# Kernel optimization log

Hardware: AMD Instinct MI355X
Metric: run time of the kernel (lower is better)

## Reference

```python
import jax, jax.numpy as jnp
import numpy as np

EPS = 1e-5

def conv1x1(x, W, b):
    # x: (B,C,H,W), W: (O,C), b: (O,)
    return jnp.einsum('bchw,oc->bohw', x, W) + b[None, :, None, None]

def setup_inputs() -> dict:
    key = jax.random.key(0)
    ks = jax.random.split(key, 16)
    B, C_in, C1, D, K, H, Wd = 8, 512, 256, 128, 32, 96, 96
    s = lambda k, shape, fan: jax.random.normal(k, shape, jnp.float32) * (1.0 / np.sqrt(fan))
    return {
        'X': jax.random.normal(ks[0], (B, C_in, H, Wd), jnp.float32),
        'W_theta': s(ks[1], (C1, C_in), C_in), 'b_theta': jnp.zeros((C1,), jnp.float32),
        'W_phi': s(ks[2], (C1, C_in), C_in), 'b_phi': jnp.zeros((C1,), jnp.float32),
        'W_g': s(ks[3], (C1, C_in), C_in), 'b_g': jnp.zeros((C1,), jnp.float32),
        'W2': s(ks[4], (C_in, C1), C1), 'b2': jnp.zeros((C_in,), jnp.float32),
        'W3': s(ks[5], (D, C_in), C_in), 'b3': jnp.zeros((D,), jnp.float32),
        'codewords': jax.random.normal(ks[6], (K, D), jnp.float32),
        'scale': -jax.random.uniform(ks[7], (K,), jnp.float32),  # Deep-TEN init: U(-1,0)
        'W_fc': s(ks[8], (C_in, D), D), 'b_fc': jnp.zeros((C_in,), jnp.float32),
    }

def reference(X, W_theta, b_theta, W_phi, b_phi, W_g, b_g, W2, b2, W3, b3,
              codewords, scale, W_fc, b_fc):
    B, C_in, H, Wd = X.shape
    C1 = W_theta.shape[0]
    D, K = W3.shape[0], codewords.shape[0]
    N = H * Wd
    # --- non-local (channel-attention) block ---
    theta = conv1x1(X, W_theta, b_theta).reshape(B, C1, N)          # (B,C1,N)
    phi = conv1x1(X, W_phi, b_phi).reshape(B, C1, N)                # (B,C1,N)
    g = conv1x1(X, W_g, b_g).reshape(B, C1, N)                      # (B,C1,N)
    f = jax.nn.softmax(jnp.einsum('bcn,bdn->bcd', theta, phi), axis=-1)  # (B,C1,C1)
    y = jnp.einsum('bcd,bdn->bcn', f, g).reshape(B, C1, H, Wd)
    z = conv1x1(y, W2, b2) + X                                      # (B,C_in,H,W)
    # --- Deep-TEN encoding ---
    z_ = conv1x1(z, W3, b3)                                         # (B,D,H,W)
    x = z_.reshape(B, D, N).transpose(0, 2, 1)                      # (B,N,D)
    # squared L2 distances to codewords without (B,N,K,D) residuals
    dist = (jnp.sum(x * x, -1, keepdims=True)
            - 2.0 * jnp.einsum('bnd,kd->bnk', x, codewords)
            + jnp.sum(codewords * codewords, -1))                   # (B,N,K)
    A = jax.nn.softmax(scale * dist, axis=-1)                       # (B,N,K)
    # E_k = sum_i A_ik (x_i - c_k)
    E = jnp.einsum('bnk,bnd->bkd', A, x) - A.sum(1)[..., None] * codewords  # (B,K,D)
    # --- training-mode batch norm over K channels (no affine) ---
    mean = E.mean(axis=(0, 2), keepdims=True)
    var = E.var(axis=(0, 2), keepdims=True)
    e = jax.nn.relu((E - mean) * jax.lax.rsqrt(var + EPS))
    Es = e.sum(axis=1)                                              # (B,D)
    gamma = jax.nn.sigmoid(Es @ W_fc.T + b_fc)                      # (B,C_in)
    return z * gamma[:, :, None, None]
```

## Files before the change

### kernel.cpp

```cpp
#include <hip/hip_runtime.h>


typedef unsigned short u16;

#define Bb 8
#define Cc 512
#define C1 256
#define Dd 128
#define Kk 32
#define Nn 9216

typedef __attribute__((ext_vector_type(8))) short short8v;
typedef __attribute__((ext_vector_type(4))) short short4v;
typedef __attribute__((ext_vector_type(4))) float f32x4;

__device__ __forceinline__ float b2f(u16 u) {
  union { unsigned int i; float f; } v; v.i = ((unsigned int)u) << 16; return v.f;
}
__device__ __forceinline__ u16 f2b(float f) {
  union { float f; unsigned int i; } v; v.f = f;
  unsigned int x = v.i;
  return (u16)((x + 0x7fffu + ((x >> 16) & 1u)) >> 16);
}

__device__ __forceinline__ float b2fOrF(float x) { return x; }
__device__ __forceinline__ float b2fOrF(u16 x) { return b2f(x); }

__device__ __forceinline__ float4 load4(const float* p) { return *(const float4*)p; }
__device__ __forceinline__ float4 load4(const u16* p) {
  ushort4 q = *(const ushort4*)p;
  return make_float4(b2f(q.x), b2f(q.y), b2f(q.z), b2f(q.w));
}
__device__ __forceinline__ void store4(float* p, float a, float b, float c, float d) {
  *(float4*)p = make_float4(a, b, c, d);
}

__device__ __forceinline__ float waveSum(float v) {
  #pragma unroll
  for (int o = 32; o > 0; o >>= 1) v += __shfl_xor(v, o);
  return v;
}
__device__ __forceinline__ float waveMax(float v) {
  #pragma unroll
  for (int o = 32; o > 0; o >>= 1) v = fmaxf(v, __shfl_xor(v, o));
  return v;
}
__device__ __forceinline__ float blockSum256(float v) {
  __shared__ float sm[4];
  v = waveSum(v);
  if ((threadIdx.x & 63) == 0) sm[threadIdx.x >> 6] = v;
  __syncthreads();
  float r = sm[0] + sm[1] + sm[2] + sm[3];
  __syncthreads();
  return r;
}
__device__ __forceinline__ float blockMax256(float v) {
  __shared__ float sm[4];
  v = waveMax(v);
  if ((threadIdx.x & 63) == 0) sm[threadIdx.x >> 6] = v;
  __syncthreads();
  float r = fmaxf(fmaxf(sm[0], sm[1]), fmaxf(sm[2], sm[3]));
  __syncthreads();
  return r;
}

__device__ __forceinline__ f32x4 mfma_bf16_16x16x32(short8v a, short8v b, f32x4 c) {
  asm("v_mfma_f32_16x16x32_bf16 %0, %1, %2, %0" : "+v"(c) : "v"(a), "v"(b));
  return c;
}

__device__ __forceinline__ int fsw(int r) { return (r ^ (r >> 2) ^ (r >> 4)) & 3; }

__device__ __forceinline__ void cvt2(float x0, float x1, unsigned int& h, unsigned int& l) {
  asm("v_cvt_pk_bf16_f32 %0, %1, %2" : "=v"(h) : "v"(x0), "v"(x1));
  union { unsigned int u; float f; } fa, fb;
  fa.u = h << 16; fb.u = h & 0xffff0000u;
  float r0 = x0 - fa.f, r1 = x1 - fb.f;
  asm("v_cvt_pk_bf16_f32 %0, %1, %2" : "=v"(l) : "v"(r0), "v"(r1));
}

__device__ __forceinline__ void storeC(float* p, float v) { *p = v; }
__device__ __forceinline__ void storeC(u16* p, float v) { *p = f2b(v); }

template<typename TO, int NF, bool TRANSB, bool ATOMIC>
__global__ __launch_bounds__(256, 2) void gemm_mfma(
    const float* __restrict__ A, const float* __restrict__ B, TO* __restrict__ C,
    int N, int K,
    long long sA, long long sB, long long sC,
    const float* __restrict__ biasRow, long long sBias,
    int kChunk, int numKS, int gnx, int gny)
{
  static_assert(NF == 4 || NF == 8, "NF");
  static_assert(!TRANSB || NF == 4, "TRANSB tile assumes BN==128");
  static_assert(!ATOMIC || __is_same(TO, float), "atomic path is fp32");
  constexpr int BN = 32 * NF;
  __shared__ __align__(16) u16 Asm_[2][128][40];
  __shared__ __align__(16) u16 Bsm_[2][BN][40];

  int id = blockIdx.x;
  {
    const int nwg = gridDim.x;
    if ((nwg & 7) == 0) id = (id & 7) * (nwg >> 3) + (id >> 3);
  }
  const int per = gnx * gny;
  const int bz = id / per;
  const int rem = id - bz * per;
  const int by = rem % gny;
  const int bx = rem / gny;
  const int b = bz / numKS, ks = bz - b * numKS;
  A += b * sA; B += b * sB; C += b * sC;
  const int m0 = by * 128, n0 = bx * BN;
  const int kBeg = ks * kChunk;
  const int kEnd = (kBeg + kChunk < K) ? (kBeg + kChunk) : K;

  const int t = threadIdx.x;
  const int w = t >> 6, lane = t & 63;
  const int wr = w >> 1, wc = w & 1;
  const int lr = lane & 15, lq = lane >> 4;

  const int sar = t >> 1, sak = (t & 1) * 16;
  const int kg = t >> 5, ng = t & 31;

  float ra[16];
  float rb[32];

  auto loadA = [&](int k0) {
    const float* p = A + (long long)(m0 + sar) * K + (k0 + sak);
    #pragma unroll
    for (int i = 0; i < 4; ++i) {
      float4 v = *(const float4*)(p + i * 4);
      ra[i*4+0] = v.x; ra[i*4+1] = v.y; ra[i*4+2] = v.z; ra[i*4+3] = v.w;
    }
  };
  auto loadB = [&](int k0) {
    if constexpr (TRANSB) {
      const float* p = B + (long long)(n0 + sar) * K + (k0 + sak);
      #pragma unroll
      for (int i = 0; i < 4; ++i) {
        float4 v = *(const float4*)(p + i * 4);
        rb[i*4+0] = v.x; rb[i*4+1] = v.y; rb[i*4+2] = v.z; rb[i*4+3] = v.w;
      }
    } else {
      const float* p = B + (long long)(k0 + kg * 4) * N + (n0 + ng * 8);
      #pragma unroll
      for (int i = 0; i < 4; ++i) {
        float4 v0 = *(const float4*)(p + (long long)i * N);
        float4 v1 = *(const float4*)(p + (long long)i * N + 4);
        rb[i*8+0]=v0.x; rb[i*8+1]=v0.y; rb[i*8+2]=v0.z; rb[i*8+3]=v0.w;
        rb[i*8+4]=v1.x; rb[i*8+5]=v1.y; rb[i*8+6]=v1.z; rb[i*8+7]=v1.w;
      }
    }
  };

  auto pack8row = [&](const float* s8, u16 (&dstH)[40], u16 (&dstL)[40], int col) {
    union { unsigned int u[4]; short8v v; } H, L;
    #pragma unroll
    for (int p = 0; p < 4; ++p) cvt2(s8[2*p], s8[2*p+1], H.u[p], L.u[p]);
    *(short8v*)&dstH[col] = H.v;
    *(short8v*)&dstL[col] = L.v;
  };

  auto stage = [&]() {
    {
      const int f = fsw(sar);
      #pragma unroll
      for (int h = 0; h < 2; ++h) {
        const int col = ((((sak >> 3) + h) ^ f) << 3);
        pack8row(&ra[h*8], Asm_[0][sar], Asm_[1][sar], col);
      }
    }
    if constexpr (TRANSB) {
      const int f = fsw(sar);
      #pragma unroll
      for (int h = 0; h < 2; ++h) {
        const int col = ((((sak >> 3) + h) ^ f) << 3);
        pack8row(&rb[h*8], Bsm_[0][sar], Bsm_[1][sar], col);
      }
    } else {
      #pragma unroll
      for (int j = 0; j < 8; ++j) {
        const int n = ng * 8 + j;
        const int col = (((kg >> 1) ^ fsw(n)) << 3) + (kg & 1) * 4;
        union { unsigned int u[2]; short4v v; } H, L;
        #pragma unroll
        for (int p = 0; p < 2; ++p)
          cvt2(rb[(2*p)*8 + j], rb[(2*p+1)*8 + j], H.u[p], L.u[p]);
        *(short4v*)&Bsm_[0][n][col] = H.v;
        *(short4v*)&Bsm_[1][n][col] = L.v;
      }
    }
  };

  f32x4 acc[4][NF];
  #pragma unroll
  for (int im = 0; im < 4; ++im)
    #pragma unroll
    for (int in = 0; in < NF; ++in)
      acc[im][in] = f32x4{0.f, 0.f, 0.f, 0.f};

  loadA(kBeg); loadB(kBeg);
  for (int k0 = kBeg; k0 < kEnd; k0 += 32) {
    stage();
    if (k0 + 32 < kEnd) { loadA(k0 + 32); loadB(k0 + 32); }
    __syncthreads();
    short8v af[2][4];
    #pragma unroll
    for (int im = 0; im < 4; ++im) {
      const int r = wr * 64 + im * 16 + lr;
      const int col = ((lq ^ fsw(r)) << 3);
      af[0][im] = *(const short8v*)&Asm_[0][r][col];
      af[1][im] = *(const short8v*)&Asm_[1][r][col];
    }
    #pragma unroll
    for (int in = 0; in < NF; ++in) {
      const int rB = wc * NF * 16 + in * 16 + lr;
      const int colB = ((lq ^ fsw(rB)) << 3);
      short8v bh = *(const short8v*)&Bsm_[0][rB][colB];
      short8v bl = *(const short8v*)&Bsm_[1][rB][colB];
      #pragma unroll
      for (int im = 0; im < 4; ++im) {
        acc[im][in] = mfma_bf16_16x16x32(af[0][im], bh, acc[im][in]);
        acc[im][in] = mfma_bf16_16x16x32(af[0][im], bl, acc[im][in]);
        acc[im][in] = mfma_bf16_16x16x32(af[1][im], bh, acc[im][in]);
      }
    }
    __syncthreads();
  }
  asm volatile("s_nop 7\n\ts_nop 7\n\ts_nop 7");

  #pragma unroll
  for (int im = 0; im < 4; ++im) {
    #pragma unroll
    for (int in = 0; in < NF; ++in) {
      const f32x4 a = acc[im][in];
      const int gc = n0 + wc * NF * 16 + in * 16 + lr;
      #pragma unroll
      for (int p = 0; p < 4; ++p) {
        const int gr = m0 + wr * 64 + im * 16 + lq * 4 + p;
        const long long idx = (long long)gr * N + gc;
        if constexpr (ATOMIC) {
          atomicAdd(&C[idx], a[p]);
        } else {
          float v = a[p];
          if (biasRow) v += biasRow[b * sBias + gr];
          storeC(&C[idx], v);
        }
      }
    }
  }
}

template<bool TRANSB>
__global__ __launch_bounds__(256) void gemm64(
    const float* __restrict__ A, const float* __restrict__ B, float* __restrict__ C,
    int M, int N, int K,
    long long sA, long long sB, long long sC,
    const float* __restrict__ biasRow, long long sBias)
{
  const int bz = blockIdx.z;
  A += (long long)bz * sA;
  B += (long long)bz * sB;
  C += (long long)bz * sC;
  const int m0 = blockIdx.y * 64, n0 = blockIdx.x * 64;
  __shared__ __align__(16) float As[16][64];
  __shared__ __align__(16) float Bs[16][64];
  const int t = threadIdx.x;
  const int lr = t >> 2, lk = (t & 3) << 2;
  const int tm = (t >> 4) << 2, tn = (t & 15) << 2;
  float acc[4][4] = {};
  for (int k0 = 0; k0 < K; k0 += 16) {
    {
      float4 a = load4(A + (long long)(m0 + lr) * K + (k0 + lk));
      As[lk + 0][lr] = a.x; As[lk + 1][lr] = a.y; As[lk + 2][lr] = a.z; As[lk + 3][lr] = a.w;
    }
    if (TRANSB) {
      float4 b = load4(B + (long long)(n0 + lr) * K + (k0 + lk));
      Bs[lk + 0][lr] = b.x; Bs[lk + 1][lr] = b.y; Bs[lk + 2][lr] = b.z; Bs[lk + 3][lr] = b.w;
    } else {
      const int kr = t >> 4, nc = (t & 15) << 2;
      float4 b = load4(B + (long long)(k0 + kr) * N + (n0 + nc));
      *(float4*)&Bs[kr][nc] = b;
    }
    __syncthreads();
    #pragma unroll
    for (int kk = 0; kk < 16; ++kk) {
      const float4 av = *(const float4*)&As[kk][tm];
      const float4 bv = *(const float4*)&Bs[kk][tn];
      acc[0][0] = fmaf(av.x, bv.x, acc[0][0]);
      acc[0][1] = fmaf(av.x, bv.y, acc[0][1]);
      acc[0][2] = fmaf(av.x, bv.z, acc[0][2]);
      acc[0][3] = fmaf(av.x, bv.w, acc[0][3]);
      acc[1][0] = fmaf(av.y, bv.x, acc[1][0]);
      acc[1][1] = fmaf(av.y, bv.y, acc[1][1]);
      acc[1][2] = fmaf(av.y, bv.z, acc[1][2]);
      acc[1][3] = fmaf(av.y, bv.w, acc[1][3]);
      acc[2][0] = fmaf(av.z, bv.x, acc[2][0]);
      acc[2][1] = fmaf(av.z, bv.y, acc[2][1]);
      acc[2][2] = fmaf(av.z, bv.z, acc[2][2]);
      acc[2][3] = fmaf(av.z, bv.w, acc[2][3]);
      acc[3][0] = fmaf(av.w, bv.x, acc[3][0]);
      acc[3][1] = fmaf(av.w, bv.y, acc[3][1]);
      acc[3][2] = fmaf(av.w, bv.z, acc[3][2]);
      acc[3][3] = fmaf(av.w, bv.w, acc[3][3]);
    }
    __syncthreads();
  }
  #pragma unroll
  for (int i = 0; i < 4; ++i) {
    const int m = m0 + tm + i;
    float bias = biasRow ? biasRow[bz * sBias + m] : 0.f;
    store4(C + (long long)m * N + (n0 + tn),
           acc[i][0] + bias, acc[i][1] + bias, acc[i][2] + bias, acc[i][3] + bias);
  }
}

__global__ __launch_bounds__(256) void rowsum_kernel(const float* __restrict__ X,
                                                     float* __restrict__ s, int N) {
  long long row = blockIdx.x;
  const float* p = X + row * N;
  float acc = 0.f;
  for (int i = threadIdx.x; i < N; i += 256) acc += p[i];
  acc = blockSum256(acc);
  if (threadIdx.x == 0) s[row] = acc;
}

__global__ __launch_bounds__(256) void gemv512_kernel(const float* __restrict__ W,
                                                      const float* __restrict__ s,
                                                      float* __restrict__ out) {
  int b = blockIdx.x;
  __shared__ float ssm[Cc];
  for (int i = threadIdx.x; i < Cc; i += 256) ssm[i] = s[b * Cc + i];
  __syncthreads();
  int i = threadIdx.x;
  const float* wr = W + i * Cc;
  float acc = 0.f;
  for (int k = 0; k < Cc; ++k) acc = fmaf(wr[k], ssm[k], acc);
  out[b * C1 + i] = acc;
}

__global__ __launch_bounds__(256) void softmax_kernel(float* __restrict__ L,
    const float* __restrict__ bth, const float* __restrict__ bph,
    const float* __restrict__ u, const float* __restrict__ v) {
  int row = blockIdx.x;
  int b = row >> 8, i = row & 255;
  int j = threadIdx.x;
  float bt = bth[i], bp = bph[j];
  long long idx = (long long)row * C1 + j;
  float val = L[idx] + bt * v[b * C1 + j] + u[b * C1 + i] * bp + (float)Nn * bt * bp;
  float mx = blockMax256(val);
  float p = expf(val - mx);
  float sm = blockSum256(p);
  L[idx] = p / sm;
}

__global__ __launch_bounds__(256) void w_kernel(const float* __restrict__ f,
                                                const float* __restrict__ bg,
                                                float* __restrict__ w) {
  int b = blockIdx.x;
  __shared__ float bgs[C1];
  bgs[threadIdx.x] = bg[threadIdx.x];
  __syncthreads();
  int i = threadIdx.x;
  const float* fr = f + ((long long)b * C1 + i) * C1;
  float acc = 0.f;
  for (int j = 0; j < C1; ++j) acc = fmaf(fr[j], bgs[j], acc);
  w[b * C1 + i] = acc;
}

__global__ __launch_bounds__(256) void q_kernel(const float* __restrict__ W2,
                                                const float* __restrict__ b2v,
                                                const float* __restrict__ w,
                                                float* __restrict__ q) {
  int gi = blockIdx.x * 256 + threadIdx.x;
  int b = gi >> 9, c = gi & 511;
  __shared__ float wsm[C1];
  wsm[threadIdx.x] = w[b * C1 + threadIdx.x];
  __syncthreads();
  const float* wr = W2 + c * C1;
  float acc = b2v[c];
  for (int i = 0; i < C1; ++i) acc = fmaf(wr[i], wsm[i], acc);
  q[gi] = acc;
}

__global__ __launch_bounds__(256) void adddiag_kernel(float* __restrict__ P) {
  int gi = blockIdx.x * 256 + threadIdx.x;
  int b = gi >> 9, c = gi & 511;
  P[((long long)b * Cc + c) * Cc + c] += 1.f;
}

__global__ __launch_bounds__(256) void zqbias_kernel(const float* __restrict__ W3,
    const float* __restrict__ b3, const float* __restrict__ q, float* __restrict__ zqb) {
  int gi = blockIdx.x * 256 + threadIdx.x;
  int b = gi >> 7, d = gi & 127;
  const float* wr = W3 + d * Cc;
  const float* qr = q + b * Cc;
  float acc = b3[d];
  for (int c = 0; c < Cc; ++c) acc = fmaf(wr[c], qr[c], acc);
  zqb[gi] = acc;
}

template<typename ZT>
__global__ __launch_bounds__(256) void enc_kernel(
    const ZT* __restrict__ zq,
    const float* __restrict__ cw,
    const float* __restrict__ sc,
    float* __restrict__ Eraw,
    float* __restrict__ Asum)
{
  __shared__ float csm[Kk][Dd + 1];
  __shared__ float cc[Kk], ssm[Kk];
  __shared__ float sA[Kk][256 + 1];
  __shared__ float zs[Dd][17];
  const int tid = threadIdx.x;
  const int b = blockIdx.y;
  const int n0 = blockIdx.x * 256;

  #pragma unroll
  for (int r = 0; r < 16; ++r) {
    int idx = r * 256 + tid;
    csm[idx >> 7][idx & 127] = cw[idx];
  }
  if (tid < Kk) ssm[tid] = sc[tid];
  __syncthreads();
  if (tid < Kk) {
    float a = 0.f;
    for (int d = 0; d < Dd; ++d) { float cv = csm[tid][d]; a = fmaf(cv, cv, a); }
    cc[tid] = a;
  }
  __syncthreads();

  const int n = n0 + tid;
  const ZT* zp = zq + (long long)b * Dd * Nn + n;
  float dots[Kk];
  #pragma unroll
  for (int k = 0; k < Kk; ++k) dots[k] = 0.f;
  float xx = 0.f;
  for (int d = 0; d < Dd; ++d) {
    float xv = b2fOrF(zp[(long long)d * Nn]);
    xx = fmaf(xv, xv, xx);
    #pragma unroll
    for (int k = 0; k < Kk; ++k) dots[k] = fmaf(csm[k][d], xv, dots[k]);
  }
  float mx = -1e30f;
  #pragma unroll
  for (int k = 0; k < Kk; ++k) {
    float l = ssm[k] * (xx - 2.f * dots[k] + cc[k]);
    dots[k] = l;
    mx = fmaxf(mx, l);
  }
  float sum = 0.f;
  #pragma unroll
  for (int k = 0; k < Kk; ++k) { float p = expf(dots[k] - mx); dots[k] = p; sum += p; }
  float inv = 1.f / sum;
  #pragma unroll
  for (int k = 0; k < Kk; ++k) sA[k][tid] = dots[k] * inv;
  __syncthreads();
  if (tid < Kk) {
    float s = 0.f;
    for (int p = 0; p < 256; ++p) s += sA[tid][p];
    atomicAdd(&Asum[b * Kk + tid], s);
  }

  float acc[16];
  #pragma unroll
  for (int j = 0; j < 16; ++j) acc[j] = 0.f;
  const int k = tid & 31, d0 = (tid >> 5) * 16;
  const int ldd = tid >> 1, lpx = (tid & 1) * 8;
  for (int it = 0; it < 16; ++it) {
    __syncthreads();
    {
      const ZT* src = zq + ((long long)b * Dd + ldd) * Nn + n0 + it * 16 + lpx;
      float4 a4 = load4(src);
      float4 b4 = load4(src + 4);
      zs[ldd][lpx + 0] = a4.x; zs[ldd][lpx + 1] = a4.y;
      zs[ldd][lpx + 2] = a4.z; zs[ldd][lpx + 3] = a4.w;
      zs[ldd][lpx + 4] = b4.x; zs[ldd][lpx + 5] = b4.y;
      zs[ldd][lpx + 6] = b4.z; zs[ldd][lpx + 7] = b4.w;
    }
    __syncthreads();
    #pragma unroll
    for (int p = 0; p < 16; ++p) {
      float a = sA[k][it * 16 + p];
      #pragma unroll
      for (int j = 0; j < 16; ++j) acc[j] = fmaf(a, zs[d0 + j][p], acc[j]);
    }
  }
  float* Ep = Eraw + ((long long)b * Kk + k) * Dd + d0;
  #pragma unroll
  for (int j = 0; j < 16; ++j) atomicAdd(Ep + j, acc[j]);
}

__global__ __launch_bounds__(256) void bn_kernel(const float* __restrict__ Eraw,
    const float* __restrict__ Asum, const float* __restrict__ cw, float* __restrict__ Es) {
  int k = blockIdx.x, tid = threadIdx.x;
  float vals[4], s = 0.f, s2 = 0.f;
  #pragma unroll
  for (int r = 0; r < 4; ++r) {
    int i = r * 256 + tid;
    int b = i >> 7, d = i & 127;
    float e = Eraw[((long long)b * Kk + k) * Dd + d] - Asum[b * Kk + k] * cw[k * Dd + d];
    vals[r] = e; s += e; s2 = fmaf(e, e, s2);
  }
  s = blockSum256(s);
  s2 = blockSum256(s2);
  float mean = s * (1.f / 1024.f);
  float var = fmaxf(s2 * (1.f / 1024.f) - mean * mean, 0.f);
  float rs = rsqrtf(var + 1e-5f);
  #pragma unroll
  for (int r = 0; r < 4; ++r) {
    int i = r * 256 + tid;
    int b = i >> 7, d = i & 127;
    float e = (vals[r] - mean) * rs;
    if (e > 0.f) atomicAdd(&Es[b * Dd + d], e);
  }
}

__global__ __launch_bounds__(256) void gamma_kernel(const float* __restrict__ Es,
    const float* __restrict__ Wfc, const float* __restrict__ bfc, float* __restrict__ gam) {
  int gi = blockIdx.x * 256 + threadIdx.x;
  int b = gi >> 9, c = gi & 511;
  __shared__ float esm[Dd];
  if (threadIdx.x < Dd) esm[threadIdx.x] = Es[b * Dd + threadIdx.x];
  __syncthreads();
  const float* wr = Wfc + c * Dd;
  float acc = bfc[c];
  for (int d = 0; d < Dd; ++d) acc = fmaf(wr[d], esm[d], acc);
  gam[gi] = 1.f / (1.f + expf(-acc));
}

__global__ __launch_bounds__(256) void scaleout_f32(float* __restrict__ out,
    const float* __restrict__ gam) {
  unsigned int idx = blockIdx.x * 256u + threadIdx.x;
  unsigned int f = idx * 4u;
  unsigned int bc = f / (unsigned)Nn;
  float g = gam[bc];
  float4 zv = *(const float4*)(out + f);
  store4(out + f, zv.x * g, zv.y * g, zv.z * g, zv.w * g);
}

extern "C" void kernel_launch(void* const* d_in, const int* in_sizes, int n_in,
                              void* d_out, int out_size, void* d_ws, size_t ws_size,
                              hipStream_t stream) {
  const float* X   = (const float*)d_in[0];
  const float* Wth = (const float*)d_in[1];
  const float* bth = (const float*)d_in[2];
  const float* Wph = (const float*)d_in[3];
  const float* bph = (const float*)d_in[4];
  const float* Wg  = (const float*)d_in[5];
  const float* bg  = (const float*)d_in[6];
  const float* W2  = (const float*)d_in[7];
  const float* b2v = (const float*)d_in[8];
  const float* W3  = (const float*)d_in[9];
  const float* b3v = (const float*)d_in[10];
  const float* CW  = (const float*)d_in[11];
  const float* SC  = (const float*)d_in[12];
  const float* Wfc = (const float*)d_in[13];
  const float* bfc = (const float*)d_in[14];
  float* out = (float*)d_out;
  float* wsf = (float*)d_ws;

  const long long szL   = (long long)Bb * C1 * C1;
  const long long szRA  = (long long)Bb * Cc * Cc;
  const long long szRB  = (long long)Bb * C1 * Cc;
  long long off = 0;
  float* s_   = wsf + off; off += Bb * Cc;
  float* u_   = wsf + off; off += Bb * C1;
  float* v_   = wsf + off; off += Bb * C1;
  float* w_   = wsf + off; off += Bb * C1;
  float* q_   = wsf + off; off += Bb * Cc;
  float* Eraw_= wsf + off; off += (long long)Bb * Kk * Dd;
  float* Es_  = wsf + off; off += Bb * Dd;
  float* Asum_= wsf + off; off += Bb * Kk;
  float* gam_ = wsf + off; off += Bb * Cc;
  float* L_   = wsf + off; off += szL;
  float* regA = wsf + off; off += szRA;
  float* regB = wsf + off; off += szRB;
  const long long baseFloats = off;
  float* tail = wsf + off;
  const long long T_STR = (long long)C1 * Nn;
  const long long ZQ_F  = (long long)Bb * Dd * Nn;
  const long long tailFloats = (long long)(ws_size / 4) - baseFloats;
  const bool big = tailFloats >= ZQ_F;
  const int grp = big ? 4 : 2;
  float* Tbuf = tail;
  float* zqf  = tail;
  u16*   zqh  = (u16*)tail;
  float* R_   = L_;
  float* zqb_ = u_;

  const long long strX = (long long)Cc * Nn;
  const long long sG = (long long)Cc * Cc;
  const long long sU = (long long)C1 * Cc;
  const long long sL = (long long)C1 * C1;
  const long long sR = (long long)Dd * Cc;

  rowsum_kernel<<<Bb * Cc, 256, 0, stream>>>(X, s_, Nn);
  hipMemsetAsync(regB, 0, (size_t)szRB * 4, stream);
  for (int g = 0; g < Bb; g += grp) {
    gemm_mfma<float, 8, false, false><<<dim3(36 * 2 * grp), 256, 0, stream>>>(
        Wth, X + (long long)g * strX, Tbuf, Nn, Cc, 0, strX, T_STR,
        nullptr, 0, Cc, 1, 36, 2);
    gemm_mfma<float, 4, true, true><<<dim3(4 * 2 * grp * 8), 256, 0, stream>>>(
        Tbuf, X + (long long)g * strX, regB + (long long)g * sU, Cc, Nn,
        T_STR, strX, sU, nullptr, 0, Nn / 8, 8, 4, 2);
  }
  gemv512_kernel<<<Bb, 256, 0, stream>>>(Wth, s_, u_);
  gemv512_kernel<<<Bb, 256, 0, stream>>>(Wph, s_, v_);
  gemm64<true><<<dim3(4, 4, Bb), 256, 0, stream>>>(
      regB, Wph, L_, C1, C1, Cc, sU, 0, sL, nullptr, 0);
  softmax_kernel<<<Bb * C1, 256, 0, stream>>>(L_, bth, bph, u_, v_);
  w_kernel<<<Bb, 256, 0, stream>>>(L_, bg, w_);
  gemm64<false><<<dim3(8, 4, Bb), 256, 0, stream>>>(
      L_, Wg, regB, C1, Cc, C1, sL, 0, sU, nullptr, 0);
  q_kernel<<<16, 256, 0, stream>>>(W2, b2v, w_, q_);
  gemm64<false><<<dim3(8, 8, Bb), 256, 0, stream>>>(
      W2, regB, regA, Cc, Cc, C1, 0, sU, sG, nullptr, 0);
  adddiag_kernel<<<16, 256, 0, stream>>>(regA);
  gemm64<false><<<dim3(8, 2, Bb), 256, 0, stream>>>(
      W3, regA, R_, Dd, Cc, Cc, 0, sG, sR, nullptr, 0);
  zqbias_kernel<<<4, 256, 0, stream>>>(W3, b3v, q_, zqb_);
  gemm_mfma<float, 8, false, false><<<dim3(1152), 256, 0, stream>>>(
      regA, X, out, Nn, Cc, sG, strX, strX, q_, Cc, Cc, 1, 36, 4);
  hipMemsetAsync(Eraw_, 0, (size_t)(Bb * Kk * Dd + Bb * Dd + Bb * Kk) * 4, stream);
  if (big) {
    gemm_mfma<float, 8, false, false><<<dim3(288), 256, 0, stream>>>(
        R_, X, zqf, Nn, Cc, sR, strX, (long long)Dd * Nn, zqb_, Dd, Cc, 1, 36, 1);
    enc_kernel<float><<<dim3(36, Bb), 256, 0, stream>>>(zqf, CW, SC, Eraw_, Asum_);
  } else {
    gemm_mfma<u16, 8, false, false><<<dim3(288), 256, 0, stream>>>(
        R_, X, zqh, Nn, Cc, sR, strX, (long long)Dd * Nn, zqb_, Dd, Cc, 1, 36, 1);
    enc_kernel<u16><<<dim3(36, Bb), 256, 0, stream>>>(zqh, CW, SC, Eraw_, Asum_);
  }
  bn_kernel<<<Kk, 256, 0, stream>>>(Eraw_, Asum_, CW, Es_);
  gamma_kernel<<<16, 256, 0, stream>>>(Es_, Wfc, bfc, gam_);
  const unsigned int n4 = (unsigned)(Bb * Cc * Nn / 4);
  scaleout_f32<<<n4 / 256, 256, 0, stream>>>(out, gam_);
  (void)in_sizes; (void)n_in; (void)out_size;
}
```

Measured before the change: 1.120 ms.

## Compute Gram matrix X·Xᵀ with symmetric split-K tiles instead of Wθ·X·Xᵀ

The old path first formed Wθ·X, a (C1,N) intermediate per batch group, and then multiplied it by Xᵀ using atomic split-K. The new path computes the per-batch Gram matrix X·Xᵀ (512x512) directly. It evaluates only the 10 upper-triangular 128x128 tile pairs with split-K partials, then reduces and mirrors them in a separate kernel, and finishes with a small GEMM by Wθ. This exploits symmetry, drops the large intermediate write and read as well as the atomics, and removes the batch-group loop. In exchange it adds a partials buffer and a reduction pass. Diagonal tiles reuse the A shared-memory tile for B.

```diff
diff --git a/kernel.cpp b/kernel.cpp
--- a/kernel.cpp
+++ b/kernel.cpp
@@ -82,17 +82,15 @@
 __device__ __forceinline__ void storeC(float* p, float v) { *p = v; }
 __device__ __forceinline__ void storeC(u16* p, float v) { *p = f2b(v); }
 
-template<typename TO, int NF, bool TRANSB, bool ATOMIC>
+template<typename TO, int NF>
 __global__ __launch_bounds__(256, 2) void gemm_mfma(
     const float* __restrict__ A, const float* __restrict__ B, TO* __restrict__ C,
     int N, int K,
     long long sA, long long sB, long long sC,
     const float* __restrict__ biasRow, long long sBias,
-    int kChunk, int numKS, int gnx, int gny)
+    int gnx, int gny)
 {
   static_assert(NF == 4 || NF == 8, "NF");
-  static_assert(!TRANSB || NF == 4, "TRANSB tile assumes BN==128");
-  static_assert(!ATOMIC || __is_same(TO, float), "atomic path is fp32");
   constexpr int BN = 32 * NF;
   __shared__ __align__(16) u16 Asm_[2][128][40];
   __shared__ __align__(16) u16 Bsm_[2][BN][40];
@@ -103,15 +101,12 @@
     if ((nwg & 7) == 0) id = (id & 7) * (nwg >> 3) + (id >> 3);
   }
   const int per = gnx * gny;
-  const int bz = id / per;
-  const int rem = id - bz * per;
+  const int b = id / per;
+  const int rem = id - b * per;
   const int by = rem % gny;
   const int bx = rem / gny;
-  const int b = bz / numKS, ks = bz - b * numKS;
   A += b * sA; B += b * sB; C += b * sC;
   const int m0 = by * 128, n0 = bx * BN;
-  const int kBeg = ks * kChunk;
-  const int kEnd = (kBeg + kChunk < K) ? (kBeg + kChunk) : K;
 
   const int t = threadIdx.x;
   const int w = t >> 6, lane = t & 63;
@@ -133,31 +128,14 @@
     }
   };
   auto loadB = [&](int k0) {
-    if constexpr (TRANSB) {
-      const float* p = B + (long long)(n0 + sar) * K + (k0 + sak);
-      #pragma unroll
-      for (int i = 0; i < 4; ++i) {
-        float4 v = *(const float4*)(p + i * 4);
-        rb[i*4+0] = v.x; rb[i*4+1] = v.y; rb[i*4+2] = v.z; rb[i*4+3] = v.w;
-      }
-    } else {
-      const float* p = B + (long long)(k0 + kg * 4) * N + (n0 + ng * 8);
-      #pragma unroll
-      for (int i = 0; i < 4; ++i) {
-        float4 v0 = *(const float4*)(p + (long long)i * N);
-        float4 v1 = *(const float4*)(p + (long long)i * N + 4);
-        rb[i*8+0]=v0.x; rb[i*8+1]=v0.y; rb[i*8+2]=v0.z; rb[i*8+3]=v0.w;
-        rb[i*8+4]=v1.x; rb[i*8+5]=v1.y; rb[i*8+6]=v1.z; rb[i*8+7]=v1.w;
-      }
-    }
-  };
-
-  auto pack8row = [&](const float* s8, u16 (&dstH)[40], u16 (&dstL)[40], int col) {
-    union { unsigned int u[4]; short8v v; } H, L;
-    #pragma unroll
-    for (int p = 0; p < 4; ++p) cvt2(s8[2*p], s8[2*p+1], H.u[p], L.u[p]);
-    *(short8v*)&dstH[col] = H.v;
-    *(short8v*)&dstL[col] = L.v;
+    const float* p = B + (long long)(k0 + kg * 4) * N + (n0 + ng * 8);
+    #pragma unroll
+    for (int i = 0; i < 4; ++i) {
+      float4 v0 = *(const float4*)(p + (long long)i * N);
+      float4 v1 = *(const float4*)(p + (long long)i * N + 4);
+      rb[i*8+0]=v0.x; rb[i*8+1]=v0.y; rb[i*8+2]=v0.z; rb[i*8+3]=v0.w;
+      rb[i*8+4]=v1.x; rb[i*8+5]=v1.y; rb[i*8+6]=v1.z; rb[i*8+7]=v1.w;
+    }
   };
 
   auto stage = [&]() {
@@ -166,17 +144,14 @@
       #pragma unroll
       for (int h = 0; h < 2; ++h) {
         const int col = ((((sak >> 3) + h) ^ f) << 3);
-        pack8row(&ra[h*8], Asm_[0][sar], Asm_[1][sar], col);
+        union { unsigned int u[4]; short8v v; } H, L;
+        #pragma unroll
+        for (int p = 0; p < 4; ++p) cvt2(ra[h*8+2*p], ra[h*8+2*p+1], H.u[p], L.u[p]);
+        *(short8v*)&Asm_[0][sar][col] = H.v;
+        *(short8v*)&Asm_[1][sar][col] = L.v;
       }
     }
-    if constexpr (TRANSB) {
-      const int f = fsw(sar);
-      #pragma unroll
-      for (int h = 0; h < 2; ++h) {
-        const int col = ((((sak >> 3) + h) ^ f) << 3);
-        pack8row(&rb[h*8], Bsm_[0][sar], Bsm_[1][sar], col);
-      }
-    } else {
+    {
       #pragma unroll
       for (int j = 0; j < 8; ++j) {
         const int n = ng * 8 + j;
@@ -198,10 +173,10 @@
     for (int in = 0; in < NF; ++in)
       acc[im][in] = f32x4{0.f, 0.f, 0.f, 0.f};
 
-  loadA(kBeg); loadB(kBeg);
-  for (int k0 = kBeg; k0 < kEnd; k0 += 32) {
+  loadA(0); loadB(0);
+  for (int k0 = 0; k0 < K; k0 += 32) {
     stage();
-    if (k0 + 32 < kEnd) { loadA(k0 + 32); loadB(k0 + 32); }
+    if (k0 + 32 < K) { loadA(k0 + 32); loadB(k0 + 32); }
     __syncthreads();
     short8v af[2][4];
     #pragma unroll
@@ -237,14 +212,159 @@
       #pragma unroll
       for (int p = 0; p < 4; ++p) {
         const int gr = m0 + wr * 64 + im * 16 + lq * 4 + p;
-        const long long idx = (long long)gr * N + gc;
-        if constexpr (ATOMIC) {
-          atomicAdd(&C[idx], a[p]);
-        } else {
-          float v = a[p];
-          if (biasRow) v += biasRow[b * sBias + gr];
-          storeC(&C[idx], v);
-        }
+        float v = a[p];
+        if (biasRow) v += biasRow[b * sBias + gr];
+        storeC(&C[(long long)gr * N + gc], v);
+      }
+    }
+  }
+}
+
+__device__ __constant__ int PIa[10] = {0,0,0,0,1,1,1,2,2,3};
+__device__ __constant__ int PJa[10] = {0,1,2,3,1,2,3,2,3,3};
+
+__global__ __launch_bounds__(256, 2) void gxxt_kernel(
+    const float* __restrict__ X, float* __restrict__ part,
+    int numKS, int kChunk)
+{
+  __shared__ __align__(16) u16 Asm_[2][128][40];
+  __shared__ __align__(16) u16 Bsm_[2][128][40];
+
+  int id = blockIdx.x;
+  {
+    const int nwg = gridDim.x;
+    if ((nwg & 7) == 0) id = (id & 7) * (nwg >> 3) + (id >> 3);
+  }
+  const int pair = id % 10;
+  const int rest = id / 10;
+  const int ks = rest % numKS;
+  const int b = rest / numKS;
+  const int i0 = PIa[pair] * 128, j0 = PJa[pair] * 128;
+  const bool same = (i0 == j0);
+  const float* Xb = X + (long long)b * Cc * Nn;
+  const int kBeg = ks * kChunk, kEnd = kBeg + kChunk;
+
+  const int t = threadIdx.x;
+  const int w = t >> 6, lane = t & 63;
+  const int wr = w >> 1, wc = w & 1;
+  const int lr = lane & 15, lq = lane >> 4;
+  const int sar = t >> 1, sak = (t & 1) * 16;
+
+  float ra[16], rb[16];
+
+  auto loadA = [&](int k0) {
+    const float* p = Xb + (long long)(i0 + sar) * Nn + (k0 + sak);
+    #pragma unroll
+    for (int i = 0; i < 4; ++i) {
+      float4 v = *(const float4*)(p + i * 4);
+      ra[i*4+0] = v.x; ra[i*4+1] = v.y; ra[i*4+2] = v.z; ra[i*4+3] = v.w;
+    }
+  };
+  auto loadB = [&](int k0) {
+    const float* p = Xb + (long long)(j0 + sar) * Nn + (k0 + sak);
+    #pragma unroll
+    for (int i = 0; i < 4; ++i) {
+      float4 v = *(const float4*)(p + i * 4);
+      rb[i*4+0] = v.x; rb[i*4+1] = v.y; rb[i*4+2] = v.z; rb[i*4+3] = v.w;
+    }
+  };
+  auto stageRow = [&](const float* s16, u16 (*H)[40], u16 (*L)[40]) {
+    const int f = fsw(sar);
+    #pragma unroll
+    for (int h = 0; h < 2; ++h) {
+      const int col = ((((sak >> 3) + h) ^ f) << 3);
+      union { unsigned int u[4]; short8v v; } Hv, Lv;
+      #pragma unroll
+      for (int p = 0; p < 4; ++p) cvt2(s16[h*8+2*p], s16[h*8+2*p+1], Hv.u[p], Lv.u[p]);
+      *(short8v*)&H[sar][col] = Hv.v;
+      *(short8v*)&L[sar][col] = Lv.v;
+    }
+  };
+
+  const u16 (*BH)[40] = same ? Asm_[0] : Bsm_[0];
+  const u16 (*BL)[40] = same ? Asm_[1] : Bsm_[1];
+
+  f32x4 acc[4][4];
+  #pragma unroll
+  for (int im = 0; im < 4; ++im)
+    #pragma unroll
+    for (int in = 0; in < 4; ++in)
+      acc[im][in] = f32x4{0.f, 0.f, 0.f, 0.f};
+
+  loadA(kBeg);
+  if (!same) loadB(kBeg);
+  for (int k0 = kBeg; k0 < kEnd; k0 += 32) {
+    stageRow(ra, Asm_[0], Asm_[1]);
+    if (!same) stageRow(rb, Bsm_[0], Bsm_[1]);
+    if (k0 + 32 < kEnd) { loadA(k0 + 32); if (!same) loadB(k0 + 32); }
+    __syncthreads();
+    short8v af[2][4];
+    #pragma unroll
+    for (int im = 0; im < 4; ++im) {
+      const int r = wr * 64 + im * 16 + lr;
+      const int col = ((lq ^ fsw(r)) << 3);
+      af[0][im] = *(const short8v*)&Asm_[0][r][col];
+      af[1][im] = *(const short8v*)&Asm_[1][r][col];
+    }
+    #pragma unroll
+    for (int in = 0; in < 4; ++in) {
+      const int rB = wc * 64 + in * 16 + lr;
+      const int colB = ((lq ^ fsw(rB)) << 3);
+      short8v bh = *(const short8v*)&BH[rB][colB];
+      short8v bl = *(const short8v*)&BL[rB][colB];
+      #pragma unroll
+      for (int im = 0; im < 4; ++im) {
+        acc[im][in] = mfma_bf16_16x16x32(af[0][im], bh, acc[im][in]);
+        acc[im][in] = mfma_bf16_16x16x32(af[0][im], bl, acc[im][in]);
+        acc[im][in] = mfma_bf16_16x16x32(af[1][im], bh, acc[im][in]);
+      }
+    }
+    __syncthreads();
+  }
+  asm volatile("s_nop 7\n\ts_nop 7\n\ts_nop 7");
+
+  float* Cp = part + ((long long)(ks * Bb + b) * 10 + pair) * 16384;
+  #pragma unroll
+  for (int im = 0; im < 4; ++im) {
+    #pragma unroll
+    for (int in = 0; in < 4; ++in) {
+      const f32x4 a = acc[im][in];
+      const int gc = wc * 64 + in * 16 + lr;
+      #pragma unroll
+      for (int p = 0; p < 4; ++p) {
+        const int gr = wr * 64 + im * 16 + lq * 4 + p;
+        Cp[gr * 128 + gc] = a[p];
+      }
+    }
+  }
+}
+
+__global__ __launch_bounds__(256) void gred_kernel(const float* __restrict__ part,
+    float* __restrict__ G, int numKS) {
+  __shared__ float sm[64][129];
+  const int pair = blockIdx.x % 10, b = blockIdx.x / 10;
+  const int i0 = PIa[pair] * 128, j0 = PJa[pair] * 128;
+  float* Gb = G + (long long)b * Cc * Cc;
+  const long long ksStr = (long long)Bb * 10 * 16384;
+  const float* p0 = part + ((long long)b * 10 + pair) * 16384;
+  const int t = threadIdx.x;
+  for (int half = 0; half < 2; ++half) {
+    const int r0 = half * 64;
+    __syncthreads();
+    for (int rep = 0; rep < 32; ++rep) {
+      int idx = r0 * 128 + rep * 256 + t;
+      float s = 0.f;
+      for (int ks = 0; ks < numKS; ++ks) s += p0[(long long)ks * ksStr + idx];
+      int r = (idx >> 7) - r0, c = idx & 127;
+      sm[r][c] = s;
+      Gb[(long long)(i0 + r0 + r) * Cc + (j0 + c)] = s;
+    }
+    if (i0 != j0) {
+      __syncthreads();
+      for (int rep = 0; rep < 32; ++rep) {
+        int o = rep * 256 + t;
+        int rr = o >> 6, cc = o & 63;
+        Gb[(long long)(j0 + rr) * Cc + (i0 + r0 + cc)] = sm[cc][rr];
       }
     }
   }
@@ -577,12 +697,11 @@
   float* regB = wsf + off; off += szRB;
   const long long baseFloats = off;
   float* tail = wsf + off;
-  const long long T_STR = (long long)C1 * Nn;
   const long long ZQ_F  = (long long)Bb * Dd * Nn;
   const long long tailFloats = (long long)(ws_size / 4) - baseFloats;
   const bool big = tailFloats >= ZQ_F;
-  const int grp = big ? 4 : 2;
-  float* Tbuf = tail;
+  const int numKS = big ? 6 : 2;
+  float* part = tail;
   float* zqf  = tail;
   u16*   zqh  = (u16*)tail;
   float* R_   = L_;
@@ -595,15 +714,10 @@
   const long long sR = (long long)Dd * Cc;
 
   rowsum_kernel<<<Bb * Cc, 256, 0, stream>>>(X, s_, Nn);
-  hipMemsetAsync(regB, 0, (size_t)szRB * 4, stream);
-  for (int g = 0; g < Bb; g += grp) {
-    gemm_mfma<float, 8, false, false><<<dim3(36 * 2 * grp), 256, 0, stream>>>(
-        Wth, X + (long long)g * strX, Tbuf, Nn, Cc, 0, strX, T_STR,
-        nullptr, 0, Cc, 1, 36, 2);
-    gemm_mfma<float, 4, true, true><<<dim3(4 * 2 * grp * 8), 256, 0, stream>>>(
-        Tbuf, X + (long long)g * strX, regB + (long long)g * sU, Cc, Nn,
-        T_STR, strX, sU, nullptr, 0, Nn / 8, 8, 4, 2);
-  }
+  gxxt_kernel<<<dim3(10 * numKS * Bb), 256, 0, stream>>>(X, part, numKS, Nn / numKS);
+  gred_kernel<<<dim3(10 * Bb), 256, 0, stream>>>(part, regA, numKS);
+  gemm64<false><<<dim3(8, 4, Bb), 256, 0, stream>>>(
+      Wth, regA, regB, C1, Cc, Cc, 0, sG, sU, nullptr, 0);
   gemv512_kernel<<<Bb, 256, 0, stream>>>(Wth, s_, u_);
   gemv512_kernel<<<Bb, 256, 0, stream>>>(Wph, s_, v_);
   gemm64<true><<<dim3(4, 4, Bb), 256, 0, stream>>>(
@@ -619,16 +733,16 @@
   gemm64<false><<<dim3(8, 2, Bb), 256, 0, stream>>>(
       W3, regA, R_, Dd, Cc, Cc, 0, sG, sR, nullptr, 0);
   zqbias_kernel<<<4, 256, 0, stream>>>(W3, b3v, q_, zqb_);
-  gemm_mfma<float, 8, false, false><<<dim3(1152), 256, 0, stream>>>(
-      regA, X, out, Nn, Cc, sG, strX, strX, q_, Cc, Cc, 1, 36, 4);
+  gemm_mfma<float, 8><<<dim3(1152), 256, 0, stream>>>(
+      regA, X, out, Nn, Cc, sG, strX, strX, q_, Cc, 36, 4);
   hipMemsetAsync(Eraw_, 0, (size_t)(Bb * Kk * Dd + Bb * Dd + Bb * Kk) * 4, stream);
   if (big) {
-    gemm_mfma<float, 8, false, false><<<dim3(288), 256, 0, stream>>>(
-        R_, X, zqf, Nn, Cc, sR, strX, (long long)Dd * Nn, zqb_, Dd, Cc, 1, 36, 1);
+    gemm_mfma<float, 8><<<dim3(288), 256, 0, stream>>>(
+        R_, X, zqf, Nn, Cc, sR, strX, (long long)Dd * Nn, zqb_, Dd, 36, 1);
     enc_kernel<float><<<dim3(36, Bb), 256, 0, stream>>>(zqf, CW, SC, Eraw_, Asum_);
   } else {
-    gemm_mfma<u16, 8, false, false><<<dim3(288), 256, 0, stream>>>(
-        R_, X, zqh, Nn, Cc, sR, strX, (long long)Dd * Nn, zqb_, Dd, Cc, 1, 36, 1);
+    gemm_mfma<u16, 8><<<dim3(288), 256, 0, stream>>>(
+        R_, X, zqh, Nn, Cc, sR, strX, (long long)Dd * Nn, zqb_, Dd, 36, 1);
     enc_kernel<u16><<<dim3(36, Bb), 256, 0, stream>>>(zqh, CW, SC, Eraw_, Asum_);
   }
   bn_kernel<<<Kk, 256, 0, stream>>>(Eraw_, Asum_, CW, Es_);
```

New measurement: 1.099 ms. No clear change (-1.9%).
